# Performance work log

Measured on AMD Instinct MI355X. Metric: run time of the kernel, lower is better.

Reference implementation:

```python
import jax, jax.numpy as jnp
import numpy as np
from jax import lax

NEG = -1.0e30  # finite stand-in for -inf (keeps vjp NaN-free)


def _ctc_losses(log_probs, input_lengths, targets, target_lengths, blank=0):
    """Per-sequence CTC negative log-likelihood (Graves 2006 forward algorithm).

    log_probs: (B,T,V) log-softmax outputs; targets: (B,U) padded labels (no blanks).
    Matches torch.nn.functional.ctc_loss(..., reduction='none') semantics per sequence.
    """
    B, T, V = log_probs.shape
    U = targets.shape[1]
    S = 2 * U + 1
    s = jnp.arange(S)
    tgt_idx = jnp.clip((s - 1) // 2, 0, U - 1)
    # Blank-interleaved extended label sequence: b, y1, b, y2, ..., yU, b
    ext = jnp.where((s % 2) == 0, blank, targets[:, tgt_idx])  # (B,S)
    ext_m2 = jnp.concatenate([jnp.full((B, 2), blank, ext.dtype), ext[:, :-2]], axis=1)
    can_skip = (ext != blank) & (ext != ext_m2) & (s >= 2)[None, :]
    idx = jnp.broadcast_to(ext[:, None, :], (B, T, S))
    lp_ext = jnp.take_along_axis(log_probs, idx, axis=2)  # (B,T,S)

    alpha0 = jnp.full((B, S), NEG, log_probs.dtype)
    alpha0 = alpha0.at[:, 0].set(lp_ext[:, 0, 0]).at[:, 1].set(lp_ext[:, 0, 1])
    neg1 = jnp.full((B, 1), NEG, log_probs.dtype)
    neg2 = jnp.full((B, 2), NEG, log_probs.dtype)

    def step(alpha, inp):
        lp_t, t = inp
        a1 = jnp.concatenate([neg1, alpha[:, :-1]], axis=1)
        a2 = jnp.concatenate([neg2, alpha[:, :-2]], axis=1)
        a2 = jnp.where(can_skip, a2, NEG)
        new = jnp.logaddexp(jnp.logaddexp(alpha, a1), a2) + lp_t
        # freeze alpha once past this sequence's input length
        alpha = jnp.where((t < input_lengths)[:, None], new, alpha)
        return alpha, None

    lp_seq = jnp.transpose(lp_ext[:, 1:, :], (1, 0, 2))  # (T-1,B,S)
    alpha, _ = lax.scan(step, alpha0, (lp_seq, jnp.arange(1, T)))
    end = 2 * target_lengths  # index of final blank in extended sequence
    a_blank = jnp.take_along_axis(alpha, end[:, None], axis=1)[:, 0]
    a_label = jnp.take_along_axis(alpha, jnp.maximum(end - 1, 0)[:, None], axis=1)[:, 0]
    return -jnp.logaddexp(a_blank, a_label)  # (B,)


def setup_inputs() -> dict:
    key = jax.random.key(0)
    k1, k2, k3, k4, k5, k6 = jax.random.split(key, 6)
    N, T, C, V, U = 16, 1000, 512, 2000, 100
    # Two augmented views of the same N utterances, stacked along batch (cr-ctc)
    enc_half = jax.random.normal(k1, (N, T, C), dtype=jnp.float32)
    encoder_out = jnp.concatenate(
        [enc_half, enc_half + 0.1 * jax.random.normal(k2, (N, T, C), dtype=jnp.float32)], axis=0)
    lens_half = jax.random.randint(k3, (N,), T // 2, T + 1, dtype=jnp.int32)
    encoder_out_lens = jnp.concatenate([lens_half, lens_half])
    tgt_half = jax.random.randint(k4, (N, U), 1, V, dtype=jnp.int32)  # labels in [1,V), 0 = blank
    targets = jnp.concatenate([tgt_half, tgt_half], axis=0)
    tl_half = jax.random.randint(k5, (N,), U // 2, U + 1, dtype=jnp.int32)
    target_lengths = jnp.concatenate([tl_half, tl_half])
    W = jax.random.normal(k6, (V, C), dtype=jnp.float32) * np.float32(1.0 / np.sqrt(C))
    b = jnp.zeros((V,), dtype=jnp.float32)
    return {"encoder_out": encoder_out, "W": W, "b": b,
            "encoder_out_lens": encoder_out_lens, "targets": targets,
            "target_lengths": target_lengths}


def reference(encoder_out, W, b, encoder_out_lens, targets, target_lengths):
    # ctc_output head: (Dropout is identity in eval) Linear -> LogSoftmax
    B, T, C = encoder_out.shape
    logits = jnp.einsum('btc,vc->btv', encoder_out, W) + b
    log_probs = jax.nn.log_softmax(logits, axis=-1)  # (B,T,V)
    # CTC loss, reduction='sum'
    ctc_loss = jnp.sum(_ctc_losses(log_probs, encoder_out_lens, targets, target_lengths))
    # Consistency regularization: KL(input=log p || target=log q), log_target=True,
    # q = detached log-probs of the swapped batch halves
    half = B // 2
    q = lax.stop_gradient(jnp.concatenate([log_probs[half:], log_probs[:half]], axis=0))
    kl = jnp.exp(q) * (q - log_probs)
    pad = (jnp.arange(T)[None, :] >= encoder_out_lens[:, None])[:, :, None]  # make_pad_mask
    cr_loss = jnp.sum(jnp.where(pad, 0.0, kl))
    return (0.5 * ctc_loss, 0.5 * cr_loss)
```

## Files before the change

kernel.cpp:

```cpp
#include <hip/hip_runtime.h>
#include <hip/hip_bf16.h>
#include <cstdint>

#define NEG (-1.0e30f)
#define INVLN2 1.44269504088896340736f
#define LN2    0.69314718055994530942f

typedef unsigned short u16;
typedef __attribute__((ext_vector_type(8))) short short8;
typedef __attribute__((ext_vector_type(4))) float f32x4;

typedef const __attribute__((address_space(1))) void cg_void;
typedef __attribute__((address_space(3))) void lds_void;

#define Bsz   32
#define Tlen  1000
#define Cdim  512
#define Vdim  2000
#define Udim  100
#define Mrows (Bsz * Tlen)
#define Npad  2048
#define GROW  256

#define WS_ABF 0u
#define WS_G   0u
#define WS_WBF 32768000u
#define WS_KL  WS_WBF
#define WS_Z   (WS_WBF + 2097152u)
#define WS_ACC (WS_Z + 128000000u)

__device__ inline u16 f2bf(float x) {
  uint32_t u = __float_as_uint(x);
  uint32_t r = (u + 0x7fffu + ((u >> 16) & 1u)) >> 16;
  return (u16)r;
}
__device__ inline float bf2f(u16 u) {
  return __uint_as_float(((uint32_t)u) << 16);
}

#define DPP_MAX_STAGE(m, ctrl) { \
    int _r = __builtin_amdgcn_update_dpp(__float_as_int(m), __float_as_int(m), \
                                         ctrl, 0xF, 0xF, false); \
    m = fmaxf(m, __int_as_float(_r)); }
#define DPP_SUM_STAGE(v, ctrl) { \
    int _r = __builtin_amdgcn_update_dpp(0, __float_as_int(v), \
                                         ctrl, 0xF, 0xF, true); \
    v += __int_as_float(_r); }

__device__ inline float dppMax64(float m) {
  DPP_MAX_STAGE(m, 0x111) DPP_MAX_STAGE(m, 0x112) DPP_MAX_STAGE(m, 0x114)
  DPP_MAX_STAGE(m, 0x118) DPP_MAX_STAGE(m, 0x142) DPP_MAX_STAGE(m, 0x143)
  return m;
}
__device__ inline float dppSum64(float v) {
  DPP_SUM_STAGE(v, 0x111) DPP_SUM_STAGE(v, 0x112) DPP_SUM_STAGE(v, 0x114)
  DPP_SUM_STAGE(v, 0x118) DPP_SUM_STAGE(v, 0x142) DPP_SUM_STAGE(v, 0x143)
  return v;
}

__device__ inline float shiftup1(float x, float fill) {
  int r = __builtin_amdgcn_update_dpp(__float_as_int(fill), __float_as_int(x),
                                      0x138, 0xF, 0xF, false);
  return __int_as_float(r);
}

__global__ void convert_kernel(const float4* __restrict__ enc4, const float4* __restrict__ W4,
                               uint4* __restrict__ a4, uint4* __restrict__ w4,
                               const int* __restrict__ lens,
                               float* __restrict__ accum) {
  int idx = blockIdx.x * blockDim.x + threadIdx.x;
  int stride = gridDim.x * blockDim.x;
  if (idx == 0) { accum[0] = 0.0f; accum[1] = 0.0f; }
  const int nA = Mrows * Cdim / 8;
  const int nW = Vdim * Cdim / 8;
  const int nWp = Npad * Cdim / 8;
  for (int i = idx; i < nA; i += stride) {
    int row = i >> 6;
    int b = row / 1000;
    int t = row - b * 1000;
    if (t >= lens[b]) continue;
    float4 x = enc4[2 * i], y = enc4[2 * i + 1];
    uint4 o;
    o.x = (uint32_t)f2bf(x.x) | ((uint32_t)f2bf(x.y) << 16);
    o.y = (uint32_t)f2bf(x.z) | ((uint32_t)f2bf(x.w) << 16);
    o.z = (uint32_t)f2bf(y.x) | ((uint32_t)f2bf(y.y) << 16);
    o.w = (uint32_t)f2bf(y.z) | ((uint32_t)f2bf(y.w) << 16);
    a4[i] = o;
  }
  for (int i = idx; i < nWp; i += stride) {
    uint4 o = {0, 0, 0, 0};
    if (i < nW) {
      float4 x = W4[2 * i], y = W4[2 * i + 1];
      o.x = (uint32_t)f2bf(x.x) | ((uint32_t)f2bf(x.y) << 16);
      o.y = (uint32_t)f2bf(x.z) | ((uint32_t)f2bf(x.w) << 16);
      o.z = (uint32_t)f2bf(y.x) | ((uint32_t)f2bf(y.y) << 16);
      o.w = (uint32_t)f2bf(y.z) | ((uint32_t)f2bf(y.w) << 16);
    }
    w4[i] = o;
  }
}

__global__ __launch_bounds__(256) void gemm_kernel(const u16* __restrict__ A,
                                                   const u16* __restrict__ Wb,
                                                   const int* __restrict__ lens,
                                                   u16* __restrict__ Z) {
  const int id = blockIdx.x;
  const int c = id >> 7, r = id & 127;
  int mTile, nTile;
  if (c < 31) { mTile = c * 8 + (r & 7); nTile = r >> 3; }
  else        { mTile = 248 + (r & 1);   nTile = r >> 1; }
  const int mBase = mTile * 128;
  const int nBase = nTile * 128;
  {
    int bSeq = mBase / 1000;
    int t0 = mBase - bSeq * 1000;
    if (t0 <= 872 && t0 >= lens[bSeq]) return;
  }

  __shared__ __attribute__((aligned(16))) u16 As[128 * 64];
  __shared__ __attribute__((aligned(16))) u16 Bs[128 * 64];
  const int tid = threadIdx.x;
  const int wave = tid >> 6;
  const int lane = tid & 63;
  const int m_lane = lane & 15;
  const int quad = lane >> 4;

  f32x4 acc[4][4];
  const f32x4 zero4 = {0.0f, 0.0f, 0.0f, 0.0f};
  #pragma unroll
  for (int i = 0; i < 4; ++i)
    #pragma unroll
    for (int j = 0; j < 4; ++j) acc[i][j] = zero4;

  for (int k0 = 0; k0 < Cdim; k0 += 64) {
    #pragma unroll
    for (int rr = 0; rr < 4; ++rr) {
      int u = rr * 256 + tid;
      int g = u >> 3;
      int q = (u & 7) ^ (g & 7);
      const u16* gpA = A + ((size_t)(mBase + g) << 9) + (k0 + (q << 3));
      __builtin_amdgcn_global_load_lds((cg_void*)gpA, (lds_void*)&As[(rr * 4 + wave) * 512],
                                       16, 0, 0);
      const u16* gpB = Wb + ((size_t)(nBase + g) << 9) + (k0 + (q << 3));
      __builtin_amdgcn_global_load_lds((cg_void*)gpB, (lds_void*)&Bs[(rr * 4 + wave) * 512],
                                       16, 0, 0);
    }
    __syncthreads();
    #pragma unroll
    for (int kk = 0; kk < 2; ++kk) {
      short8 af[4], bfv[4];
      #pragma unroll
      for (int mi = 0; mi < 4; ++mi) {
        int row = (wave >> 1) * 64 + mi * 16 + m_lane;
        int q = (kk * 4 + quad) ^ (row & 7);
        af[mi] = *(const short8*)&As[row * 64 + (q << 3)];
      }
      #pragma unroll
      for (int ni = 0; ni < 4; ++ni) {
        int col = (wave & 1) * 64 + ni * 16 + m_lane;
        int q = (kk * 4 + quad) ^ (col & 7);
        bfv[ni] = *(const short8*)&Bs[col * 64 + (q << 3)];
      }
      #pragma unroll
      for (int mi = 0; mi < 4; ++mi)
        #pragma unroll
        for (int ni = 0; ni < 4; ++ni)
          acc[mi][ni] = __builtin_amdgcn_mfma_f32_16x16x32_bf16(af[mi], bfv[ni],
                                                                acc[mi][ni], 0, 0, 0);
    }
    __syncthreads();
  }
  #pragma unroll
  for (int ni = 0; ni < 4; ++ni) {
    int col = nBase + (wave & 1) * 64 + ni * 16 + m_lane;
    if (col < Vdim) {
      #pragma unroll
      for (int mi = 0; mi < 4; ++mi) {
        int row0 = mBase + (wave >> 1) * 64 + mi * 16 + quad * 4;
        #pragma unroll
        for (int rg = 0; rg < 4; ++rg)
          Z[(size_t)(row0 + rg) * Vdim + col] = f2bf(acc[mi][ni][rg]);
      }
    }
  }
}

__global__ __launch_bounds__(256) void cr_stats_kernel(const u16* __restrict__ Z,
                                                       const float* __restrict__ bias,
                                                       const int* __restrict__ lens,
                                                       const int* __restrict__ targets,
                                                       const int* __restrict__ tlens,
                                                       float* __restrict__ G,
                                                       float* __restrict__ klp) {
  int bp = blockIdx.x;
  int t = blockIdx.y;
  int tid = threadIdx.x;
  size_t r1 = (size_t)bp * Tlen + t;
  if (t >= lens[bp]) {
    if (tid == 0) klp[r1] = 0.0f;
    return;
  }
  int wave = tid >> 6, lane = tid & 63;
  size_t r2 = r1 + (size_t)16 * Tlen;
  const u16* z1 = Z + r1 * Vdim;
  const u16* z2 = Z + r2 * Vdim;

  __shared__ __attribute__((aligned(16))) float ls1[Vdim];
  __shared__ __attribute__((aligned(16))) float ls2[Vdim];
  __shared__ float red[8];

  const int c0 = tid * 8;
  float v1[8], v2[8], e1[8], e2[8];
  float mx1 = NEG, mx2 = NEG;
  if (c0 < Vdim) {
    short8 za = *(const short8*)&z1[c0];
    short8 zb = *(const short8*)&z2[c0];
    float4 b0 = *(const float4*)&bias[c0];
    float4 b1 = *(const float4*)&bias[c0 + 4];
    float bb[8] = {b0.x, b0.y, b0.z, b0.w, b1.x, b1.y, b1.z, b1.w};
    #pragma unroll
    for (int j = 0; j < 8; ++j) {
      v1[j] = bf2f((u16)za[j]) + bb[j];
      v2[j] = bf2f((u16)zb[j]) + bb[j];
      mx1 = fmaxf(mx1, v1[j]);
      mx2 = fmaxf(mx2, v2[j]);
    }
    *(float4*)&ls1[c0]     = (float4){v1[0], v1[1], v1[2], v1[3]};
    *(float4*)&ls1[c0 + 4] = (float4){v1[4], v1[5], v1[6], v1[7]};
    *(float4*)&ls2[c0]     = (float4){v2[0], v2[1], v2[2], v2[3]};
    *(float4*)&ls2[c0 + 4] = (float4){v2[4], v2[5], v2[6], v2[7]};
  } else {
    #pragma unroll
    for (int j = 0; j < 8; ++j) { v1[j] = NEG; v2[j] = NEG; }
  }
  float w1 = dppMax64(mx1), w2 = dppMax64(mx2);
  if (lane == 63) { red[wave] = w1; red[4 + wave] = w2; }
  __syncthreads();
  float M1 = fmaxf(fmaxf(red[0], red[1]), fmaxf(red[2], red[3]));
  float M2 = fmaxf(fmaxf(red[4], red[5]), fmaxf(red[6], red[7]));
  __syncthreads();
  float s1 = 0.0f, s2 = 0.0f;
  #pragma unroll
  for (int j = 0; j < 8; ++j) {
    e1[j] = expf(v1[j] - M1);
    e2[j] = expf(v2[j] - M2);
    s1 += e1[j];
    s2 += e2[j];
  }
  s1 = dppSum64(s1); s2 = dppSum64(s2);
  if (lane == 63) { red[wave] = s1; red[4 + wave] = s2; }
  __syncthreads();
  float S1 = red[0] + red[1] + red[2] + red[3];
  float S2 = red[4] + red[5] + red[6] + red[7];
  float c1 = M1 + logf(S1);
  float c2 = M2 + logf(S2);
  float inv1 = 1.0f / S1;
  float inv2 = 1.0f / S2;

  if (tid < 64) {
    int i1 = min(2 * tid, Udim - 1);
    int i3 = min(2 * tid + 1, Udim - 1);
    int t1a = targets[bp * Udim + i1];
    int t1b = targets[bp * Udim + i3];
    int t2a = targets[(bp + 16) * Udim + i1];
    int t2b = targets[(bp + 16) * Udim + i3];
    int tl1 = tlens[bp];
    int tl2 = tlens[bp + 16];
    float4 g1 = {(2 * tid < tl1) ? expf(ls1[t1a] - c1) : 0.0f,
                 (2 * tid + 1 < tl1) ? expf(ls1[t1b] - c1) : 0.0f,
                 expf(ls1[0] - c1), 0.0f};
    float4 g2 = {(2 * tid < tl2) ? expf(ls2[t2a] - c2) : 0.0f,
                 (2 * tid + 1 < tl2) ? expf(ls2[t2b] - c2) : 0.0f,
                 expf(ls2[0] - c2), 0.0f};
    *(float4*)(G + r1 * GROW + 4 * tid) = g1;
    *(float4*)(G + r2 * GROW + 4 * tid) = g2;
  }

  float f = 0.0f;
  #pragma unroll
  for (int j = 0; j < 8; ++j) {
    float p1 = e1[j] * inv1;
    float p2 = e2[j] * inv2;
    f += (p1 - p2) * (v1[j] - v2[j]);
  }
  __syncthreads();
  f = dppSum64(f);
  if (lane == 63) red[wave] = f;
  __syncthreads();
  if (tid == 0) {
    klp[r1] = red[0] + red[1] + red[2] + red[3];
  }
}

#define DECL3(p, i) float p##i##x, p##i##y, p##i##b;
#define LOADR(p, i, row) { float4 v = *(const float4*)(gb + (size_t)(row) * GROW + 4 * lane); \
    p##i##x = v.x; p##i##y = v.y; p##i##b = v.z; }

#define COMPU(p, i) { \
    float pX = p##i##x, pY = p##i##y, pB = p##i##b; \
    float p3 = shiftup1(a3, 0.0f); \
    float t01 = a1 + a0; \
    float t23 = a3 + a2; \
    float n0 = (a0 + p3) * pB; \
    float n1 = fmaf(p3, fm1, t01) * pX; \
    float n2 = (a2 + a1) * pB; \
    float n3 = fmaf(a1, fm3, t23) * pY; \
    a0 = n0; a1 = n1; a2 = n2; a3 = n3; }

#define COMPA(p, i, off) { \
    float pX = p##i##x, pY = p##i##y, pB = p##i##b; \
    float p3 = shiftup1(a3, 0.0f); \
    float t01 = a1 + a0; \
    float t23 = a3 + a2; \
    float n0 = (a0 + p3) * pB; \
    float n1 = fmaf(p3, fm1, t01) * pX; \
    float n2 = (a2 + a1) * pB; \
    float n3 = fmaf(a1, fm3, t23) * pY; \
    bool act = (t + (off)) < len; \
    a0 = act ? n0 : a0; a1 = act ? n1 : a1; \
    a2 = act ? n2 : a2; a3 = act ? n3 : a3; }

#define DPPMAX(m, ctrl) { int _r = __builtin_amdgcn_update_dpp(0,              \
      __float_as_int(m), ctrl, 0xF, 0xF, true);                               \
    m = fmaxf(m, __int_as_float(_r)); }

#define RESCALE_KILL(tdone) {                                                 \
    int R = len - 1 - (tdone); R = R < 0 ? 0 : R;                             \
    int lo = end1 - 2 * R;                                                    \
    a0 = (base4 + 0 >= lo) ? a0 : 0.0f;                                       \
    a1 = (base4 + 1 >= lo) ? a1 : 0.0f;                                       \
    a2 = (base4 + 2 >= lo) ? a2 : 0.0f;                                       \
    a3 = (base4 + 3 >= lo) ? a3 : 0.0f;                                       \
    float m = fmaxf(fmaxf(a0, a1), fmaxf(a2, a3));                            \
    DPPMAX(m, 0x111) DPPMAX(m, 0x112) DPPMAX(m, 0x114) DPPMAX(m, 0x118)       \
    DPPMAX(m, 0x142) DPPMAX(m, 0x143)                                         \
    uint32_t mb = (uint32_t)__builtin_amdgcn_readlane(__float_as_int(m), 63); \
    int e = (int)((mb >> 23) & 0xffu);                                        \
    int sh = 227 - e;                                                         \
    sh = sh > 127 ? 127 : (sh < -126 ? -126 : sh);                            \
    float sc = __uint_as_float((uint32_t)(sh + 127) << 23);                   \
    a0 *= sc; a1 *= sc; a2 *= sc; a3 *= sc;                                   \
    logScale -= sh; }

__global__ __launch_bounds__(64, 1) void ctc_kernel(const float* __restrict__ G,
                                                    const int* __restrict__ targets,
                                                    const int* __restrict__ lens,
                                                    const int* __restrict__ tlens,
                                                    float* __restrict__ accum) {
  int b = blockIdx.x;
  int lane = threadIdx.x;
  const int* tgt = targets + b * Udim;
  int i1 = min(2 * lane, Udim - 1);
  int i3 = min(2 * lane + 1, Udim - 1);
  int l1 = tgt[i1];
  int l3 = tgt[i3];
  int lm1 = tgt[min(max(2 * lane - 1, 0), Udim - 1)];
  const float fm1 = ((lane >= 1) && (l1 != lm1)) ? 1.0f : 0.0f;
  const float fm3 = (l3 != l1) ? 1.0f : 0.0f;
  int len = lens[b];
  int tl = tlens[b];
  const int end1 = 2 * tl - 1;
  const int base4 = 4 * lane;
  const float* gb = G + (size_t)b * Tlen * GROW;

  float4 v0 = *(const float4*)(gb + 4 * lane);
  float a0 = (lane == 0) ? v0.z : 0.0f;
  float a1 = (lane == 0) ? v0.x : 0.0f;
  float a2 = 0.0f, a3 = 0.0f;
  int logScale = 0;

  DECL3(sA, 0)  DECL3(sA, 1)  DECL3(sA, 2)  DECL3(sA, 3)
  DECL3(sA, 4)  DECL3(sA, 5)  DECL3(sA, 6)  DECL3(sA, 7)
  DECL3(sA, 8)  DECL3(sA, 9)  DECL3(sA, 10) DECL3(sA, 11)
  DECL3(sA, 12) DECL3(sA, 13) DECL3(sA, 14) DECL3(sA, 15)
  DECL3(sB, 0)  DECL3(sB, 1)  DECL3(sB, 2)  DECL3(sB, 3)
  DECL3(sB, 4)  DECL3(sB, 5)  DECL3(sB, 6)  DECL3(sB, 7)
  DECL3(sB, 8)  DECL3(sB, 9)  DECL3(sB, 10) DECL3(sB, 11)
  DECL3(sB, 12) DECL3(sB, 13) DECL3(sB, 14) DECL3(sB, 15)

  LOADR(sA, 0, 1)   LOADR(sA, 1, 2)   LOADR(sA, 2, 3)   LOADR(sA, 3, 4)
  LOADR(sA, 4, 5)   LOADR(sA, 5, 6)   LOADR(sA, 6, 7)   LOADR(sA, 7, 8)
  LOADR(sA, 8, 9)   LOADR(sA, 9, 10)  LOADR(sA, 10, 11) LOADR(sA, 11, 12)
  LOADR(sA, 12, 13) LOADR(sA, 13, 14) LOADR(sA, 14, 15) LOADR(sA, 15, 16)

  int steps = len - 1;
  int mainN = steps & ~31;
  int t = 1;
  for (int blk = 0; blk < mainN; blk += 32) {
    LOADR(sB, 0, t + 16)  LOADR(sB, 1, t + 17)  LOADR(sB, 2, t + 18)  LOADR(sB, 3, t + 19)
    LOADR(sB, 4, t + 20)  LOADR(sB, 5, t + 21)  LOADR(sB, 6, t + 22)  LOADR(sB, 7, t + 23)
    LOADR(sB, 8, t + 24)  LOADR(sB, 9, t + 25)  LOADR(sB, 10, t + 26) LOADR(sB, 11, t + 27)
    LOADR(sB, 12, t + 28) LOADR(sB, 13, t + 29) LOADR(sB, 14, t + 30) LOADR(sB, 15, t + 31)
    __builtin_amdgcn_sched_barrier(0);
    COMPU(sA, 0)  COMPU(sA, 1)  COMPU(sA, 2)  COMPU(sA, 3)
    COMPU(sA, 4)  COMPU(sA, 5)  COMPU(sA, 6)  COMPU(sA, 7)
    RESCALE_KILL(t + 7)
    COMPU(sA, 8)  COMPU(sA, 9)  COMPU(sA, 10) COMPU(sA, 11)
    COMPU(sA, 12) COMPU(sA, 13) COMPU(sA, 14) COMPU(sA, 15)
    RESCALE_KILL(t + 15)
    LOADR(sA, 0, t + 32)  LOADR(sA, 1, t + 33)  LOADR(sA, 2, t + 34)  LOADR(sA, 3, t + 35)
    LOADR(sA, 4, t + 36)  LOADR(sA, 5, t + 37)  LOADR(sA, 6, t + 38)  LOADR(sA, 7, t + 39)
    LOADR(sA, 8, t + 40)  LOADR(sA, 9, t + 41)  LOADR(sA, 10, t + 42) LOADR(sA, 11, t + 43)
    LOADR(sA, 12, t + 44) LOADR(sA, 13, t + 45) LOADR(sA, 14, t + 46) LOADR(sA, 15, t + 47)
    __builtin_amdgcn_sched_barrier(0);
    COMPU(sB, 0)  COMPU(sB, 1)  COMPU(sB, 2)  COMPU(sB, 3)
    COMPU(sB, 4)  COMPU(sB, 5)  COMPU(sB, 6)  COMPU(sB, 7)
    RESCALE_KILL(t + 23)
    COMPU(sB, 8)  COMPU(sB, 9)  COMPU(sB, 10) COMPU(sB, 11)
    COMPU(sB, 12) COMPU(sB, 13) COMPU(sB, 14) COMPU(sB, 15)
    RESCALE_KILL(t + 31)
    t += 32;
  }
  {
    LOADR(sB, 0, t + 16)  LOADR(sB, 1, t + 17)  LOADR(sB, 2, t + 18)  LOADR(sB, 3, t + 19)
    LOADR(sB, 4, t + 20)  LOADR(sB, 5, t + 21)  LOADR(sB, 6, t + 22)  LOADR(sB, 7, t + 23)
    LOADR(sB, 8, t + 24)  LOADR(sB, 9, t + 25)  LOADR(sB, 10, t + 26) LOADR(sB, 11, t + 27)
    LOADR(sB, 12, t + 28) LOADR(sB, 13, t + 29) LOADR(sB, 14, t + 30) LOADR(sB, 15, t + 31)
    __builtin_amdgcn_sched_barrier(0);
    COMPA(sA, 0, 0)   COMPA(sA, 1, 1)   COMPA(sA, 2, 2)   COMPA(sA, 3, 3)
    COMPA(sA, 4, 4)   COMPA(sA, 5, 5)   COMPA(sA, 6, 6)   COMPA(sA, 7, 7)
    RESCALE_KILL(t + 7)
    COMPA(sA, 8, 8)   COMPA(sA, 9, 9)   COMPA(sA, 10, 10) COMPA(sA, 11, 11)
    COMPA(sA, 12, 12) COMPA(sA, 13, 13) COMPA(sA, 14, 14) COMPA(sA, 15, 15)
    RESCALE_KILL(t + 15)
    COMPA(sB, 0, 16)  COMPA(sB, 1, 17)  COMPA(sB, 2, 18)  COMPA(sB, 3, 19)
    COMPA(sB, 4, 20)  COMPA(sB, 5, 21)  COMPA(sB, 6, 22)  COMPA(sB, 7, 23)
    RESCALE_KILL(t + 23)
    COMPA(sB, 8, 24)  COMPA(sB, 9, 25)  COMPA(sB, 10, 26) COMPA(sB, 11, 27)
    COMPA(sB, 12, 28) COMPA(sB, 13, 29) COMPA(sB, 14, 30) COMPA(sB, 15, 31)
    RESCALE_KILL(t + 31)
  }

  __shared__ float fin[256];
  fin[4 * lane + 0] = a0;
  fin[4 * lane + 1] = a1;
  fin[4 * lane + 2] = a2;
  fin[4 * lane + 3] = a3;
  __syncthreads();
  if (lane == 0) {
    int end = 2 * tl;
    float sum = fin[end] + fin[end - 1];
    float loss = -LN2 * (log2f(sum) + (float)logScale);
    atomicAdd(&accum[0], 0.5f * loss);
  }
}

__global__ __launch_bounds__(1024) void finalize_kernel(const float* __restrict__ accum,
                                                        const float* __restrict__ klp,
                                                        float* __restrict__ out) {
  __shared__ float red[16];
  int tid = threadIdx.x;
  float s = 0.0f;
  for (int i = tid; i < 16 * Tlen; i += 1024) s += klp[i];
  s = dppSum64(s);
  int wave = tid >> 6, lane = tid & 63;
  if (lane == 63) red[wave] = s;
  __syncthreads();
  if (tid == 0) {
    float tot = 0.0f;
    #pragma unroll
    for (int w = 0; w < 16; ++w) tot += red[w];
    out[0] = accum[0];
    out[1] = 0.5f * tot;
  }
}

extern "C" void kernel_launch(void* const* d_in, const int* in_sizes, int n_in,
                              void* d_out, int out_size, void* d_ws, size_t ws_size,
                              hipStream_t stream) {
  const float* enc = (const float*)d_in[0];
  const float* W = (const float*)d_in[1];
  const float* bias = (const float*)d_in[2];
  const int* lens = (const int*)d_in[3];
  const int* targets = (const int*)d_in[4];
  const int* tlens = (const int*)d_in[5];

  char* ws = (char*)d_ws;
  u16* a_bf = (u16*)(ws + WS_ABF);
  u16* w_bf = (u16*)(ws + WS_WBF);
  u16* Zb   = (u16*)(ws + WS_Z);
  float* Gp  = (float*)(ws + WS_G);
  float* klp = (float*)(ws + WS_KL);
  float* accum = (float*)(ws + WS_ACC);

  hipLaunchKernelGGL(convert_kernel, dim3(1024), dim3(256), 0, stream,
                     (const float4*)enc, (const float4*)W, (uint4*)a_bf, (uint4*)w_bf,
                     lens, accum);
  hipLaunchKernelGGL(gemm_kernel, dim3(4000), dim3(256), 0, stream,
                     a_bf, w_bf, lens, Zb);
  hipLaunchKernelGGL(cr_stats_kernel, dim3(16, 1000), dim3(256), 0, stream,
                     Zb, bias, lens, targets, tlens, Gp, klp);
  hipLaunchKernelGGL(ctc_kernel, dim3(Bsz), dim3(64), 0, stream,
                     Gp, targets, lens, tlens, accum);
  hipLaunchKernelGGL(finalize_kernel, dim3(1), dim3(1024), 0, stream,
                     accum, klp, (float*)d_out);
}
```

Before: 289.7 us.

## Widen GEMM tile to 128x256 with 8 waves and triple-buffered LDS pipeline

The logits GEMM now uses 512-thread blocks computing 128x256 tiles, with eight waves arranged 2x4. Global-to-LDS loads are triple-buffered and issued two k-steps ahead, with vmcnt waits replacing the per-iteration full syncthreads, and MFMA sections run under raised wave priority. The aim is to hide load latency and cut barrier stalls, and the wider N tile means each A tile is reused more often. In exchange it uses more LDS per block (72 KB), which may limit occupancy, and the new block-index mapping must cover the padded N correctly.

```diff
diff --git a/kernel.cpp b/kernel.cpp
--- a/kernel.cpp
+++ b/kernel.cpp
@@ -100,30 +100,49 @@
   }
 }
 
-__global__ __launch_bounds__(256) void gemm_kernel(const u16* __restrict__ A,
+__global__ __launch_bounds__(512) void gemm_kernel(const u16* __restrict__ A,
                                                    const u16* __restrict__ Wb,
                                                    const int* __restrict__ lens,
                                                    u16* __restrict__ Z) {
   const int id = blockIdx.x;
   const int c = id >> 7, r = id & 127;
   int mTile, nTile;
-  if (c < 31) { mTile = c * 8 + (r & 7); nTile = r >> 3; }
-  else        { mTile = 248 + (r & 1);   nTile = r >> 1; }
+  if (c < 15) { mTile = c * 16 + (r & 15); nTile = r >> 4; }
+  else        { mTile = 240 + (r % 10);    nTile = r / 10; }
   const int mBase = mTile * 128;
-  const int nBase = nTile * 128;
+  const int nBase = nTile * 256;
   {
     int bSeq = mBase / 1000;
     int t0 = mBase - bSeq * 1000;
     if (t0 <= 872 && t0 >= lens[bSeq]) return;
   }
 
-  __shared__ __attribute__((aligned(16))) u16 As[128 * 64];
-  __shared__ __attribute__((aligned(16))) u16 Bs[128 * 64];
+  __shared__ __attribute__((aligned(16))) u16 As[3][128 * 64];
+  __shared__ __attribute__((aligned(16))) u16 Bs[3][256 * 64];
   const int tid = threadIdx.x;
-  const int wave = tid >> 6;
+  const int wid = tid >> 6;
   const int lane = tid & 63;
+  const int wm = wid >> 2;
+  const int wn = wid & 3;
   const int m_lane = lane & 15;
   const int quad = lane >> 4;
+
+  auto STAGE_A = [&](int kt, int s, int l) {
+    int u = l * 512 + tid;
+    int g = u >> 3;
+    int q = (u & 7) ^ (g & 7);
+    const u16* gp = A + ((size_t)(mBase + g) << 9) + (kt * 64 + (q << 3));
+    __builtin_amdgcn_global_load_lds((cg_void*)gp, (lds_void*)&As[s][(l * 8 + wid) * 512],
+                                     16, 0, 0);
+  };
+  auto STAGE_B = [&](int kt, int s, int l) {
+    int u = l * 512 + tid;
+    int g = u >> 3;
+    int q = (u & 7) ^ (g & 7);
+    const u16* gp = Wb + ((size_t)(nBase + g) << 9) + (kt * 64 + (q << 3));
+    __builtin_amdgcn_global_load_lds((cg_void*)gp, (lds_void*)&Bs[s][(l * 8 + wid) * 512],
+                                     16, 0, 0);
+  };
 
   f32x4 acc[4][4];
   const f32x4 zero4 = {0.0f, 0.0f, 0.0f, 0.0f};
@@ -132,51 +151,83 @@
     #pragma unroll
     for (int j = 0; j < 4; ++j) acc[i][j] = zero4;
 
-  for (int k0 = 0; k0 < Cdim; k0 += 64) {
-    #pragma unroll
-    for (int rr = 0; rr < 4; ++rr) {
-      int u = rr * 256 + tid;
-      int g = u >> 3;
-      int q = (u & 7) ^ (g & 7);
-      const u16* gpA = A + ((size_t)(mBase + g) << 9) + (k0 + (q << 3));
-      __builtin_amdgcn_global_load_lds((cg_void*)gpA, (lds_void*)&As[(rr * 4 + wave) * 512],
-                                       16, 0, 0);
-      const u16* gpB = Wb + ((size_t)(nBase + g) << 9) + (k0 + (q << 3));
-      __builtin_amdgcn_global_load_lds((cg_void*)gpB, (lds_void*)&Bs[(rr * 4 + wave) * 512],
-                                       16, 0, 0);
-    }
-    __syncthreads();
-    #pragma unroll
-    for (int kk = 0; kk < 2; ++kk) {
-      short8 af[4], bfv[4];
+  STAGE_A(0, 0, 0); STAGE_A(0, 0, 1);
+  STAGE_B(0, 0, 0); STAGE_B(0, 0, 1); STAGE_B(0, 0, 2); STAGE_B(0, 0, 3);
+  STAGE_A(1, 1, 0); STAGE_A(1, 1, 1);
+  STAGE_B(1, 1, 0); STAGE_B(1, 1, 1); STAGE_B(1, 1, 2); STAGE_B(1, 1, 3);
+  asm volatile("s_waitcnt vmcnt(6)" ::: "memory");
+  __builtin_amdgcn_s_barrier();
+  asm volatile("" ::: "memory");
+
+  #pragma unroll
+  for (int t = 0; t < 8; ++t) {
+    const int s = t % 3;
+    const int sn = (t + 2) % 3;
+    short8 af[4][2], bfv[2][2];
+    if (t < 6) { STAGE_A(t + 2, sn, 0); STAGE_A(t + 2, sn, 1); STAGE_B(t + 2, sn, 0); }
+    #pragma unroll
+    for (int mi = 0; mi < 4; ++mi) {
+      int row = wm * 64 + mi * 16 + m_lane;
       #pragma unroll
-      for (int mi = 0; mi < 4; ++mi) {
-        int row = (wave >> 1) * 64 + mi * 16 + m_lane;
+      for (int kk = 0; kk < 2; ++kk) {
         int q = (kk * 4 + quad) ^ (row & 7);
-        af[mi] = *(const short8*)&As[row * 64 + (q << 3)];
+        af[mi][kk] = *(const short8*)&As[s][row * 64 + (q << 3)];
       }
+    }
+    #pragma unroll
+    for (int ni = 0; ni < 2; ++ni) {
+      int col = wn * 64 + ni * 16 + m_lane;
       #pragma unroll
-      for (int ni = 0; ni < 4; ++ni) {
-        int col = (wave & 1) * 64 + ni * 16 + m_lane;
+      for (int kk = 0; kk < 2; ++kk) {
         int q = (kk * 4 + quad) ^ (col & 7);
-        bfv[ni] = *(const short8*)&Bs[col * 64 + (q << 3)];
+        bfv[ni][kk] = *(const short8*)&Bs[s][col * 64 + (q << 3)];
       }
+    }
+    __builtin_amdgcn_s_setprio(1);
+    #pragma unroll
+    for (int mi = 0; mi < 4; ++mi)
       #pragma unroll
-      for (int mi = 0; mi < 4; ++mi)
+      for (int ni = 0; ni < 2; ++ni)
         #pragma unroll
-        for (int ni = 0; ni < 4; ++ni)
-          acc[mi][ni] = __builtin_amdgcn_mfma_f32_16x16x32_bf16(af[mi], bfv[ni],
+        for (int kk = 0; kk < 2; ++kk)
+          acc[mi][ni] = __builtin_amdgcn_mfma_f32_16x16x32_bf16(af[mi][kk], bfv[ni][kk],
                                                                 acc[mi][ni], 0, 0, 0);
-    }
-    __syncthreads();
-  }
+    __builtin_amdgcn_s_setprio(0);
+    if (t < 6) { STAGE_B(t + 2, sn, 1); STAGE_B(t + 2, sn, 2); STAGE_B(t + 2, sn, 3); }
+    #pragma unroll
+    for (int ni = 0; ni < 2; ++ni) {
+      int col = wn * 64 + (ni + 2) * 16 + m_lane;
+      #pragma unroll
+      for (int kk = 0; kk < 2; ++kk) {
+        int q = (kk * 4 + quad) ^ (col & 7);
+        bfv[ni][kk] = *(const short8*)&Bs[s][col * 64 + (q << 3)];
+      }
+    }
+    __builtin_amdgcn_s_setprio(1);
+    #pragma unroll
+    for (int mi = 0; mi < 4; ++mi)
+      #pragma unroll
+      for (int ni = 0; ni < 2; ++ni)
+        #pragma unroll
+        for (int kk = 0; kk < 2; ++kk)
+          acc[mi][ni + 2] = __builtin_amdgcn_mfma_f32_16x16x32_bf16(af[mi][kk], bfv[ni][kk],
+                                                                    acc[mi][ni + 2], 0, 0, 0);
+    __builtin_amdgcn_s_setprio(0);
+    if (t < 6)      { asm volatile("s_waitcnt vmcnt(6)" ::: "memory"); }
+    else if (t == 6){ asm volatile("s_waitcnt vmcnt(0)" ::: "memory"); }
+    if (t < 7) {
+      __builtin_amdgcn_s_barrier();
+      asm volatile("" ::: "memory");
+    }
+  }
+
   #pragma unroll
   for (int ni = 0; ni < 4; ++ni) {
-    int col = nBase + (wave & 1) * 64 + ni * 16 + m_lane;
+    int col = nBase + wn * 64 + ni * 16 + m_lane;
     if (col < Vdim) {
       #pragma unroll
       for (int mi = 0; mi < 4; ++mi) {
-        int row0 = mBase + (wave >> 1) * 64 + mi * 16 + quad * 4;
+        int row0 = mBase + wm * 64 + mi * 16 + quad * 4;
         #pragma unroll
         for (int rg = 0; rg < 4; ++rg)
           Z[(size_t)(row0 + rg) * Vdim + col] = f2bf(acc[mi][ni][rg]);
@@ -486,7 +537,7 @@
   hipLaunchKernelGGL(convert_kernel, dim3(1024), dim3(256), 0, stream,
                      (const float4*)enc, (const float4*)W, (uint4*)a_bf, (uint4*)w_bf,
                      lens, accum);
-  hipLaunchKernelGGL(gemm_kernel, dim3(4000), dim3(256), 0, stream,
+  hipLaunchKernelGGL(gemm_kernel, dim3(2000), dim3(512), 0, stream,
                      a_bf, w_bf, lens, Zb);
   hipLaunchKernelGGL(cr_stats_kernel, dim3(16, 1000), dim3(256), 0, stream,
                      Zb, bias, lens, targets, tlens, Gp, klp);
```

Result: no change. 291.9 us (+0.7%).

## Double-buffer GEMM LDS tiles and deepen CTC register prefetch to 32 steps

Applied to the files above, without the earlier changes.

The GEMM kernel now uses two LDS stages, issuing the next K-tile's global_load_lds before computing the current one. This removes one of the two barriers per K step and raises MFMA wave priority during the math. Separately, the CTC recursion kernel prefetches 32 timesteps per register buffer instead of 16, hiding more global-load latency behind the serial recursion. The cost is double LDS per GEMM block, which may lower occupancy, and much higher VGPR use in the CTC kernel, which risks spills.

```diff
diff --git a/kernel.cpp b/kernel.cpp
--- a/kernel.cpp
+++ b/kernel.cpp
@@ -117,13 +117,28 @@
     if (t0 <= 872 && t0 >= lens[bSeq]) return;
   }
 
-  __shared__ __attribute__((aligned(16))) u16 As[128 * 64];
-  __shared__ __attribute__((aligned(16))) u16 Bs[128 * 64];
+  __shared__ __attribute__((aligned(16))) u16 As[2][128 * 64];
+  __shared__ __attribute__((aligned(16))) u16 Bs[2][128 * 64];
   const int tid = threadIdx.x;
   const int wave = tid >> 6;
   const int lane = tid & 63;
   const int m_lane = lane & 15;
   const int quad = lane >> 4;
+
+  auto STAGE = [&](int k0, int s) {
+    #pragma unroll
+    for (int rr = 0; rr < 4; ++rr) {
+      int u = rr * 256 + tid;
+      int g = u >> 3;
+      int q = (u & 7) ^ (g & 7);
+      const u16* gpA = A + ((size_t)(mBase + g) << 9) + (k0 + (q << 3));
+      __builtin_amdgcn_global_load_lds((cg_void*)gpA, (lds_void*)&As[s][(rr * 4 + wave) * 512],
+                                       16, 0, 0);
+      const u16* gpB = Wb + ((size_t)(nBase + g) << 9) + (k0 + (q << 3));
+      __builtin_amdgcn_global_load_lds((cg_void*)gpB, (lds_void*)&Bs[s][(rr * 4 + wave) * 512],
+                                       16, 0, 0);
+    }
+  };
 
   f32x4 acc[4][4];
   const f32x4 zero4 = {0.0f, 0.0f, 0.0f, 0.0f};
@@ -132,20 +147,13 @@
     #pragma unroll
     for (int j = 0; j < 4; ++j) acc[i][j] = zero4;
 
-  for (int k0 = 0; k0 < Cdim; k0 += 64) {
-    #pragma unroll
-    for (int rr = 0; rr < 4; ++rr) {
-      int u = rr * 256 + tid;
-      int g = u >> 3;
-      int q = (u & 7) ^ (g & 7);
-      const u16* gpA = A + ((size_t)(mBase + g) << 9) + (k0 + (q << 3));
-      __builtin_amdgcn_global_load_lds((cg_void*)gpA, (lds_void*)&As[(rr * 4 + wave) * 512],
-                                       16, 0, 0);
-      const u16* gpB = Wb + ((size_t)(nBase + g) << 9) + (k0 + (q << 3));
-      __builtin_amdgcn_global_load_lds((cg_void*)gpB, (lds_void*)&Bs[(rr * 4 + wave) * 512],
-                                       16, 0, 0);
-    }
-    __syncthreads();
+  STAGE(0, 0);
+  __syncthreads();
+
+  #pragma unroll
+  for (int t = 0; t < 8; ++t) {
+    const int s = t & 1;
+    if (t < 7) STAGE((t + 1) * 64, s ^ 1);
     #pragma unroll
     for (int kk = 0; kk < 2; ++kk) {
       short8 af[4], bfv[4];
@@ -153,23 +161,26 @@
       for (int mi = 0; mi < 4; ++mi) {
         int row = (wave >> 1) * 64 + mi * 16 + m_lane;
         int q = (kk * 4 + quad) ^ (row & 7);
-        af[mi] = *(const short8*)&As[row * 64 + (q << 3)];
+        af[mi] = *(const short8*)&As[s][row * 64 + (q << 3)];
       }
       #pragma unroll
       for (int ni = 0; ni < 4; ++ni) {
         int col = (wave & 1) * 64 + ni * 16 + m_lane;
         int q = (kk * 4 + quad) ^ (col & 7);
-        bfv[ni] = *(const short8*)&Bs[col * 64 + (q << 3)];
+        bfv[ni] = *(const short8*)&Bs[s][col * 64 + (q << 3)];
       }
+      __builtin_amdgcn_s_setprio(1);
       #pragma unroll
       for (int mi = 0; mi < 4; ++mi)
         #pragma unroll
         for (int ni = 0; ni < 4; ++ni)
           acc[mi][ni] = __builtin_amdgcn_mfma_f32_16x16x32_bf16(af[mi], bfv[ni],
                                                                 acc[mi][ni], 0, 0, 0);
+      __builtin_amdgcn_s_setprio(0);
     }
-    __syncthreads();
-  }
+    if (t < 7) __syncthreads();
+  }
+
   #pragma unroll
   for (int ni = 0; ni < 4; ++ni) {
     int col = nBase + (wave & 1) * 64 + ni * 16 + m_lane;
@@ -342,6 +353,50 @@
     a0 *= sc; a1 *= sc; a2 *= sc; a3 *= sc;                                   \
     logScale -= sh; }
 
+#define LOAD32(p, base) \
+    LOADR(p, 0,  (base) + 0)  LOADR(p, 1,  (base) + 1)  LOADR(p, 2,  (base) + 2)  LOADR(p, 3,  (base) + 3)  \
+    LOADR(p, 4,  (base) + 4)  LOADR(p, 5,  (base) + 5)  LOADR(p, 6,  (base) + 6)  LOADR(p, 7,  (base) + 7)  \
+    LOADR(p, 8,  (base) + 8)  LOADR(p, 9,  (base) + 9)  LOADR(p, 10, (base) + 10) LOADR(p, 11, (base) + 11) \
+    LOADR(p, 12, (base) + 12) LOADR(p, 13, (base) + 13) LOADR(p, 14, (base) + 14) LOADR(p, 15, (base) + 15) \
+    LOADR(p, 16, (base) + 16) LOADR(p, 17, (base) + 17) LOADR(p, 18, (base) + 18) LOADR(p, 19, (base) + 19) \
+    LOADR(p, 20, (base) + 20) LOADR(p, 21, (base) + 21) LOADR(p, 22, (base) + 22) LOADR(p, 23, (base) + 23) \
+    LOADR(p, 24, (base) + 24) LOADR(p, 25, (base) + 25) LOADR(p, 26, (base) + 26) LOADR(p, 27, (base) + 27) \
+    LOADR(p, 28, (base) + 28) LOADR(p, 29, (base) + 29) LOADR(p, 30, (base) + 30) LOADR(p, 31, (base) + 31)
+
+#define COMPU32(p, tb) \
+    COMPU(p, 0)  COMPU(p, 1)  COMPU(p, 2)  COMPU(p, 3)  \
+    COMPU(p, 4)  COMPU(p, 5)  COMPU(p, 6)  COMPU(p, 7)  \
+    RESCALE_KILL((tb) + 7) \
+    COMPU(p, 8)  COMPU(p, 9)  COMPU(p, 10) COMPU(p, 11) \
+    COMPU(p, 12) COMPU(p, 13) COMPU(p, 14) COMPU(p, 15) \
+    RESCALE_KILL((tb) + 15) \
+    COMPU(p, 16) COMPU(p, 17) COMPU(p, 18) COMPU(p, 19) \
+    COMPU(p, 20) COMPU(p, 21) COMPU(p, 22) COMPU(p, 23) \
+    RESCALE_KILL((tb) + 23) \
+    COMPU(p, 24) COMPU(p, 25) COMPU(p, 26) COMPU(p, 27) \
+    COMPU(p, 28) COMPU(p, 29) COMPU(p, 30) COMPU(p, 31) \
+    RESCALE_KILL((tb) + 31)
+
+#define COMPA32(p, o) \
+    COMPA(p, 0,  (o) + 0)  COMPA(p, 1,  (o) + 1)  COMPA(p, 2,  (o) + 2)  COMPA(p, 3,  (o) + 3)  \
+    COMPA(p, 4,  (o) + 4)  COMPA(p, 5,  (o) + 5)  COMPA(p, 6,  (o) + 6)  COMPA(p, 7,  (o) + 7)  \
+    RESCALE_KILL(t + (o) + 7) \
+    COMPA(p, 8,  (o) + 8)  COMPA(p, 9,  (o) + 9)  COMPA(p, 10, (o) + 10) COMPA(p, 11, (o) + 11) \
+    COMPA(p, 12, (o) + 12) COMPA(p, 13, (o) + 13) COMPA(p, 14, (o) + 14) COMPA(p, 15, (o) + 15) \
+    RESCALE_KILL(t + (o) + 15) \
+    COMPA(p, 16, (o) + 16) COMPA(p, 17, (o) + 17) COMPA(p, 18, (o) + 18) COMPA(p, 19, (o) + 19) \
+    COMPA(p, 20, (o) + 20) COMPA(p, 21, (o) + 21) COMPA(p, 22, (o) + 22) COMPA(p, 23, (o) + 23) \
+    RESCALE_KILL(t + (o) + 23) \
+    COMPA(p, 24, (o) + 24) COMPA(p, 25, (o) + 25) COMPA(p, 26, (o) + 26) COMPA(p, 27, (o) + 27) \
+    COMPA(p, 28, (o) + 28) COMPA(p, 29, (o) + 29) COMPA(p, 30, (o) + 30) COMPA(p, 31, (o) + 31) \
+    RESCALE_KILL(t + (o) + 31)
+
+#define DECL32(p) \
+    DECL3(p, 0)  DECL3(p, 1)  DECL3(p, 2)  DECL3(p, 3)  DECL3(p, 4)  DECL3(p, 5)  DECL3(p, 6)  DECL3(p, 7)  \
+    DECL3(p, 8)  DECL3(p, 9)  DECL3(p, 10) DECL3(p, 11) DECL3(p, 12) DECL3(p, 13) DECL3(p, 14) DECL3(p, 15) \
+    DECL3(p, 16) DECL3(p, 17) DECL3(p, 18) DECL3(p, 19) DECL3(p, 20) DECL3(p, 21) DECL3(p, 22) DECL3(p, 23) \
+    DECL3(p, 24) DECL3(p, 25) DECL3(p, 26) DECL3(p, 27) DECL3(p, 28) DECL3(p, 29) DECL3(p, 30) DECL3(p, 31)
+
 __global__ __launch_bounds__(64, 1) void ctc_kernel(const float* __restrict__ G,
                                                     const int* __restrict__ targets,
                                                     const int* __restrict__ lens,
@@ -369,66 +424,28 @@
   float a2 = 0.0f, a3 = 0.0f;
   int logScale = 0;
 
-  DECL3(sA, 0)  DECL3(sA, 1)  DECL3(sA, 2)  DECL3(sA, 3)
-  DECL3(sA, 4)  DECL3(sA, 5)  DECL3(sA, 6)  DECL3(sA, 7)
-  DECL3(sA, 8)  DECL3(sA, 9)  DECL3(sA, 10) DECL3(sA, 11)
-  DECL3(sA, 12) DECL3(sA, 13) DECL3(sA, 14) DECL3(sA, 15)
-  DECL3(sB, 0)  DECL3(sB, 1)  DECL3(sB, 2)  DECL3(sB, 3)
-  DECL3(sB, 4)  DECL3(sB, 5)  DECL3(sB, 6)  DECL3(sB, 7)
-  DECL3(sB, 8)  DECL3(sB, 9)  DECL3(sB, 10) DECL3(sB, 11)
-  DECL3(sB, 12) DECL3(sB, 13) DECL3(sB, 14) DECL3(sB, 15)
-
-  LOADR(sA, 0, 1)   LOADR(sA, 1, 2)   LOADR(sA, 2, 3)   LOADR(sA, 3, 4)
-  LOADR(sA, 4, 5)   LOADR(sA, 5, 6)   LOADR(sA, 6, 7)   LOADR(sA, 7, 8)
-  LOADR(sA, 8, 9)   LOADR(sA, 9, 10)  LOADR(sA, 10, 11) LOADR(sA, 11, 12)
-  LOADR(sA, 12, 13) LOADR(sA, 13, 14) LOADR(sA, 14, 15) LOADR(sA, 15, 16)
+  DECL32(sA)
+  DECL32(sB)
+
+  LOAD32(sA, 1)
 
   int steps = len - 1;
-  int mainN = steps & ~31;
+  int mainN = steps & ~63;
   int t = 1;
-  for (int blk = 0; blk < mainN; blk += 32) {
-    LOADR(sB, 0, t + 16)  LOADR(sB, 1, t + 17)  LOADR(sB, 2, t + 18)  LOADR(sB, 3, t + 19)
-    LOADR(sB, 4, t + 20)  LOADR(sB, 5, t + 21)  LOADR(sB, 6, t + 22)  LOADR(sB, 7, t + 23)
-    LOADR(sB, 8, t + 24)  LOADR(sB, 9, t + 25)  LOADR(sB, 10, t + 26) LOADR(sB, 11, t + 27)
-    LOADR(sB, 12, t + 28) LOADR(sB, 13, t + 29) LOADR(sB, 14, t + 30) LOADR(sB, 15, t + 31)
+  for (int blk = 0; blk < mainN; blk += 64) {
+    LOAD32(sB, t + 32)
     __builtin_amdgcn_sched_barrier(0);
-    COMPU(sA, 0)  COMPU(sA, 1)  COMPU(sA, 2)  COMPU(sA, 3)
-    COMPU(sA, 4)  COMPU(sA, 5)  COMPU(sA, 6)  COMPU(sA, 7)
-    RESCALE_KILL(t + 7)
-    COMPU(sA, 8)  COMPU(sA, 9)  COMPU(sA, 10) COMPU(sA, 11)
-    COMPU(sA, 12) COMPU(sA, 13) COMPU(sA, 14) COMPU(sA, 15)
-    RESCALE_KILL(t + 15)
-    LOADR(sA, 0, t + 32)  LOADR(sA, 1, t + 33)  LOADR(sA, 2, t + 34)  LOADR(sA, 3, t + 35)
-    LOADR(sA, 4, t + 36)  LOADR(sA, 5, t + 37)  LOADR(sA, 6, t + 38)  LOADR(sA, 7, t + 39)
-    LOADR(sA, 8, t + 40)  LOADR(sA, 9, t + 41)  LOADR(sA, 10, t + 42) LOADR(sA, 11, t + 43)
-    LOADR(sA, 12, t + 44) LOADR(sA, 13, t + 45) LOADR(sA, 14, t + 46) LOADR(sA, 15, t + 47)
+    COMPU32(sA, t)
+    LOAD32(sA, t + 64)
     __builtin_amdgcn_sched_barrier(0);
-    COMPU(sB, 0)  COMPU(sB, 1)  COMPU(sB, 2)  COMPU(sB, 3)
-    COMPU(sB, 4)  COMPU(sB, 5)  COMPU(sB, 6)  COMPU(sB, 7)
-    RESCALE_KILL(t + 23)
-    COMPU(sB, 8)  COMPU(sB, 9)  COMPU(sB, 10) COMPU(sB, 11)
-    COMPU(sB, 12) COMPU(sB, 13) COMPU(sB, 14) COMPU(sB, 15)
-    RESCALE_KILL(t + 31)
-    t += 32;
+    COMPU32(sB, t + 32)
+    t += 64;
   }
   {
-    LOADR(sB, 0, t + 16)  LOADR(sB, 1, t + 17)  LOADR(sB, 2, t + 18)  LOADR(sB, 3, t + 19)
-    LOADR(sB, 4, t + 20)  LOADR(sB, 5, t + 21)  LOADR(sB, 6, t + 22)  LOADR(sB, 7, t + 23)
-    LOADR(sB, 8, t + 24)  LOADR(sB, 9, t + 25)  LOADR(sB, 10, t + 26) LOADR(sB, 11, t + 27)
-    LOADR(sB, 12, t + 28) LOADR(sB, 13, t + 29) LOADR(sB, 14, t + 30) LOADR(sB, 15, t + 31)
+    LOAD32(sB, t + 32)
     __builtin_amdgcn_sched_barrier(0);
-    COMPA(sA, 0, 0)   COMPA(sA, 1, 1)   COMPA(sA, 2, 2)   COMPA(sA, 3, 3)
-    COMPA(sA, 4, 4)   COMPA(sA, 5, 5)   COMPA(sA, 6, 6)   COMPA(sA, 7, 7)
-    RESCALE_KILL(t + 7)
-    COMPA(sA, 8, 8)   COMPA(sA, 9, 9)   COMPA(sA, 10, 10) COMPA(sA, 11, 11)
-    COMPA(sA, 12, 12) COMPA(sA, 13, 13) COMPA(sA, 14, 14) COMPA(sA, 15, 15)
-    RESCALE_KILL(t + 15)
-    COMPA(sB, 0, 16)  COMPA(sB, 1, 17)  COMPA(sB, 2, 18)  COMPA(sB, 3, 19)
-    COMPA(sB, 4, 20)  COMPA(sB, 5, 21)  COMPA(sB, 6, 22)  COMPA(sB, 7, 23)
-    RESCALE_KILL(t + 23)
-    COMPA(sB, 8, 24)  COMPA(sB, 9, 25)  COMPA(sB, 10, 26) COMPA(sB, 11, 27)
-    COMPA(sB, 12, 28) COMPA(sB, 13, 29) COMPA(sB, 14, 30) COMPA(sB, 15, 31)
-    RESCALE_KILL(t + 31)
+    COMPA32(sA, 0)
+    COMPA32(sB, 32)
   }
 
   __shared__ float fin[256];
```

New measurement: 283.6 us. 1.02x faster.
